# Kernel optimization log

Hardware: AMD Instinct MI355X
Metric: run time of the kernel (lower is better)

Reference implementation:

```python
import jax, jax.numpy as jnp
import numpy as np

N_NODES = 100000
N_EDGES = 3200000
F_IN, HIDDEN, NCLASS = 512, 256, 40


def setup_inputs() -> dict:
    key = jax.random.key(0)
    k1, k2, k3, k4, k5, k6 = jax.random.split(key, 6)
    x = jax.random.normal(k1, (N_NODES, F_IN), dtype=jnp.float32)
    edge_row = jax.random.randint(k2, (N_EDGES,), 0, N_NODES, dtype=jnp.int32)
    edge_col = jax.random.randint(k3, (N_EDGES,), 0, N_NODES, dtype=jnp.int32)
    edge_vals = jax.random.uniform(k4, (N_EDGES,), dtype=jnp.float32)
    stdv1 = 1.0 / np.sqrt(HIDDEN)
    stdv2 = 1.0 / np.sqrt(NCLASS)
    W1 = jax.random.uniform(k5, (F_IN, HIDDEN), minval=-stdv1, maxval=stdv1, dtype=jnp.float32)
    W2 = jax.random.uniform(k6, (HIDDEN, NCLASS), minval=-stdv2, maxval=stdv2, dtype=jnp.float32)
    return {"x": x, "edge_row": edge_row, "edge_col": edge_col,
            "edge_vals": edge_vals, "W1": W1, "W2": W2}


def _spmm(edge_row, edge_col, edge_vals, dense):
    # out[r] = sum_{edges e with row r} vals[e] * dense[col[e]]
    msgs = edge_vals[:, None] * dense[edge_col]  # [E, D]
    return jax.ops.segment_sum(msgs, edge_row, num_segments=N_NODES)


def reference(x, edge_row, edge_col, edge_vals, W1, W2):
    # Layer 1: dense projection + sparse aggregation + ReLU
    h = jax.nn.relu(_spmm(edge_row, edge_col, edge_vals, x @ W1))  # [N, HIDDEN]
    # dropout is identity in eval mode
    # Layer 2
    h = jax.nn.relu(_spmm(edge_row, edge_col, edge_vals, h @ W2))  # [N, NCLASS]
    return jax.nn.log_softmax(h, axis=1)
```

## Files before the change

kernel.cpp:

```cpp
#include <hip/hip_runtime.h>
#include <math.h>

#define N_NODES 100000
#define N_EDGES 3200000
#define F_IN    512
#define HIDDEN  256
#define NCLASS  40
#define NPAD    48
#define H2STRIDE 64
#define FB_ROWS 16
#define G1_BLOCKS ((N_NODES + 63) / 64)
#define FILL_BLOCKS (N_EDGES / 256)

#define SCAN_B  256
#define N_SCANB ((N_NODES + SCAN_B - 1) / SCAN_B)

typedef __attribute__((ext_vector_type(8))) _Float16 half8;
typedef __attribute__((ext_vector_type(4))) _Float16 half4;
typedef __attribute__((ext_vector_type(4))) float    f32x4;
typedef __attribute__((ext_vector_type(2))) float    f32x2;

__device__ __forceinline__ float unpack_val(unsigned pk) {
    unsigned short hb = (unsigned short)(pk & 0x7FFFu);
    _Float16 h = *(_Float16*)&hb;
    return (float)h;
}

__global__ __launch_bounds__(256) void init_kernel(const float* __restrict__ W1,
                                                   const float* __restrict__ W2,
                                                   _Float16* __restrict__ W1T,
                                                   _Float16* __restrict__ W2T,
                                                   int* __restrict__ deg) {
    int o = blockIdx.x * 256 + threadIdx.x;
    {
        int n = o >> 9, k = o & 511;
        W1T[o] = (_Float16)W1[(size_t)k * HIDDEN + n];
    }
    if (o < NPAD * HIDDEN) {
        int n = o >> 8, k = o & 255;
        W2T[o] = (n < NCLASS) ? (_Float16)W2[(size_t)k * NCLASS + n] : (_Float16)0.f;
    }
    if (o < N_NODES) deg[o] = 0;
}

__global__ __launch_bounds__(256) void hist2_kernel(const int* __restrict__ erow,
                                                    int* __restrict__ deg,
                                                    unsigned short* __restrict__ ke, int E) {
    int e = blockIdx.x * 256 + threadIdx.x;
    if (e < E) ke[e] = (unsigned short)atomicAdd(&deg[erow[e]], 1);
}

__global__ __launch_bounds__(256) void scanA_kernel(const int* __restrict__ deg,
                                                    int* __restrict__ rptr,
                                                    int* __restrict__ bsum, int n) {
    __shared__ int s[SCAN_B];
    int i = blockIdx.x * SCAN_B + threadIdx.x;
    int v = (i < n) ? deg[i] : 0;
    s[threadIdx.x] = v;
    __syncthreads();
    #pragma unroll
    for (int off = 1; off < SCAN_B; off <<= 1) {
        int t = (threadIdx.x >= off) ? s[threadIdx.x - off] : 0;
        __syncthreads();
        s[threadIdx.x] += t;
        __syncthreads();
    }
    if (i < n) rptr[i] = s[threadIdx.x] - v;
    if (threadIdx.x == SCAN_B - 1) bsum[blockIdx.x] = s[SCAN_B - 1];
}

__global__ __launch_bounds__(512) void scanB_kernel(int* __restrict__ bsum, int nb) {
    __shared__ int s[512];
    int t = threadIdx.x;
    int v = (t < nb) ? bsum[t] : 0;
    s[t] = v;
    __syncthreads();
    #pragma unroll
    for (int off = 1; off < 512; off <<= 1) {
        int x = (t >= off) ? s[t - off] : 0;
        __syncthreads();
        s[t] += x;
        __syncthreads();
    }
    if (t < nb) bsum[t] = s[t] - v;
}

__global__ __launch_bounds__(256) void scanC_kernel(int* __restrict__ rptr,
                                                    const int* __restrict__ bsum,
                                                    int n, int E) {
    int i = blockIdx.x * SCAN_B + threadIdx.x;
    if (i < n) rptr[i] += bsum[blockIdx.x];
    if (i == 0) rptr[n] = E;
}

__global__ __launch_bounds__(256) void fill_gemm1_kernel(
        const float* __restrict__ A, const _Float16* __restrict__ BT,
        unsigned char* __restrict__ C, int M,
        const int* __restrict__ erow, const int* __restrict__ ecol,
        const float* __restrict__ evals, const int* __restrict__ rptr,
        const unsigned short* __restrict__ ke, unsigned* __restrict__ cvp, int E) {
    __shared__ __align__(16) char smem[33792];

    if (blockIdx.x >= G1_BLOCKS) {
        int e = (blockIdx.x - G1_BLOCKS) * 256 + threadIdx.x;
        if (e < E) {
            int p = rptr[erow[e]] + ke[e];
            _Float16 h = (_Float16)evals[e];
            unsigned short hb = *(unsigned short*)&h;
            cvp[p] = ((unsigned)ecol[e] << 15) | (unsigned)(hb & 0x7FFFu);
        }
        return;
    }

    _Float16 (*As)[40]  = (_Float16 (*)[40])smem;
    _Float16 (*Bs)[40]  = (_Float16 (*)[40])(smem + 5120);
    _Float16 (*sC)[264] = (_Float16 (*)[264])smem;

    const int t    = threadIdx.x;
    const int m0   = blockIdx.x * 64;
    const int lane = t & 63;
    const int wid  = t >> 6;
    const int lr   = lane & 15, lk = lane >> 4;

    f32x4 acc[4][4] = {};

    const int  ar   = t >> 2;
    const int  aq   = t & 3;
    const bool aval = (m0 + ar) < M;
    const float*    aptr = A  + (size_t)(m0 + ar) * F_IN + aq * 8;
    const _Float16* bptr = BT + (size_t)t * F_IN;

    float4 a0 = {0.f,0.f,0.f,0.f}, a1 = {0.f,0.f,0.f,0.f};
    half8 b0, b1, b2, b3;
    if (aval) { a0 = *(const float4*)(aptr); a1 = *(const float4*)(aptr + 4); }
    { const half8* bp = (const half8*)(bptr); b0 = bp[0]; b1 = bp[1]; b2 = bp[2]; b3 = bp[3]; }

    for (int k0 = 0; k0 < F_IN; k0 += 32) {
        half8 ah;
        ah[0]=(_Float16)a0.x; ah[1]=(_Float16)a0.y; ah[2]=(_Float16)a0.z; ah[3]=(_Float16)a0.w;
        ah[4]=(_Float16)a1.x; ah[5]=(_Float16)a1.y; ah[6]=(_Float16)a1.z; ah[7]=(_Float16)a1.w;
        *(half8*)&As[ar][aq * 8] = ah;
        *(half8*)&Bs[t][0]  = b0;
        *(half8*)&Bs[t][8]  = b1;
        *(half8*)&Bs[t][16] = b2;
        *(half8*)&Bs[t][24] = b3;
        __syncthreads();

        if (k0 + 32 < F_IN) {
            if (aval) {
                a0 = *(const float4*)(aptr + k0 + 32);
                a1 = *(const float4*)(aptr + k0 + 36);
            }
            const half8* bp = (const half8*)(bptr + k0 + 32);
            b0 = bp[0]; b1 = bp[1]; b2 = bp[2]; b3 = bp[3];
        }

        half8 af[4], bf[4];
        #pragma unroll
        for (int fm = 0; fm < 4; fm++) af[fm] = *(half8*)&As[fm * 16 + lr][lk * 8];
        #pragma unroll
        for (int fn = 0; fn < 4; fn++) bf[fn] = *(half8*)&Bs[wid * 64 + fn * 16 + lr][lk * 8];
        #pragma unroll
        for (int fm = 0; fm < 4; fm++)
            #pragma unroll
            for (int fn = 0; fn < 4; fn++)
                acc[fm][fn] = __builtin_amdgcn_mfma_f32_16x16x32_f16(af[fm], bf[fn], acc[fm][fn], 0, 0, 0);
        __syncthreads();
    }

    #pragma unroll
    for (int fm = 0; fm < 4; fm++)
        #pragma unroll
        for (int fn = 0; fn < 4; fn++)
            #pragma unroll
            for (int j = 0; j < 4; j++) {
                int row = fm * 16 + lk * 4 + j;
                int col = wid * 64 + fn * 16 + lr;
                sC[row][col] = (_Float16)acc[fm][fn][j];
            }
    __syncthreads();

    int m = m0 + ar;
    if (m < M) {
        const half8* sp = (const half8*)&sC[ar][aq * 64];
        unsigned w[16];
        #pragma unroll
        for (int c = 0; c < 8; c++) {
            half8 hv = sp[c];
            unsigned lo = __builtin_amdgcn_cvt_pk_fp8_f32((float)hv[0], (float)hv[1], 0u, false);
            lo = __builtin_amdgcn_cvt_pk_fp8_f32((float)hv[2], (float)hv[3], lo, true);
            unsigned hi = __builtin_amdgcn_cvt_pk_fp8_f32((float)hv[4], (float)hv[5], 0u, false);
            hi = __builtin_amdgcn_cvt_pk_fp8_f32((float)hv[6], (float)hv[7], hi, true);
            w[c * 2]     = lo;
            w[c * 2 + 1] = hi;
        }
        uint4* dp = (uint4*)(C + (size_t)m * HIDDEN + aq * 64);
        #pragma unroll
        for (int c = 0; c < 4; c++)
            dp[c] = make_uint4(w[c*4], w[c*4+1], w[c*4+2], w[c*4+3]);
    }
}

__global__ __launch_bounds__(1024) void spmm_gemm2_kernel(const int* __restrict__ rptr,
                                                          const unsigned* __restrict__ cvp,
                                                          const unsigned char* __restrict__ H1,
                                                          const _Float16* __restrict__ W2T,
                                                          _Float16* __restrict__ H2) {
    __shared__ _Float16 sW2[NPAD][264];
    __shared__ _Float16 sRow[16][264];

    int t = threadIdx.x;
    int wave = t >> 6, lane = t & 63;
    int m0 = blockIdx.x * FB_ROWS;
    int r = m0 + wave;

    #pragma unroll
    for (int i = 0; i < 2; i++) {
        int idx = t + i * 1024;
        if (idx < NPAD * 32) {
            int row = idx >> 5, c8 = idx & 31;
            *(half8*)&sW2[row][c8 * 8] = *(const half8*)(W2T + (size_t)row * HIDDEN + c8 * 8);
        }
    }

    int e0 = rptr[r], e1 = rptr[r + 1];
    int qf = lane >> 4;
    int fl = lane & 15;

    float acc[16] = {};
    for (int e = e0; e < e1; e += 16) {
        #pragma unroll
        for (int u = 0; u < 4; u++) {
            int idx = e + 4 * u + qf;
            bool ok = idx < e1;
            unsigned pk = cvp[ok ? idx : (e1 - 1)];
            float v = ok ? unpack_val(pk) : 0.f;
            int col = (int)(pk >> 15);
            uint4 raw = *(const uint4*)(H1 + (size_t)col * HIDDEN + fl * 16);
            #pragma unroll
            for (int q = 0; q < 4; q++) {
                unsigned wq = (q == 0) ? raw.x : (q == 1) ? raw.y : (q == 2) ? raw.z : raw.w;
                f32x2 lo = __builtin_amdgcn_cvt_pk_f32_fp8(wq, false);
                f32x2 hi = __builtin_amdgcn_cvt_pk_f32_fp8(wq, true);
                acc[q*4 + 0] += v * lo[0];
                acc[q*4 + 1] += v * lo[1];
                acc[q*4 + 2] += v * hi[0];
                acc[q*4 + 3] += v * hi[1];
            }
        }
    }
    #pragma unroll
    for (int j = 0; j < 16; j++) {
        acc[j] += __shfl_xor(acc[j], 32);
        acc[j] += __shfl_xor(acc[j], 16);
    }

    if (lane < 16) {
        half8 o0, o1;
        #pragma unroll
        for (int j = 0; j < 8; j++) {
            o0[j] = (_Float16)fmaxf(acc[j], 0.f);
            o1[j] = (_Float16)fmaxf(acc[8 + j], 0.f);
        }
        *(half8*)&sRow[wave][fl * 16]     = o0;
        *(half8*)&sRow[wave][fl * 16 + 8] = o1;
    }
    __syncthreads();

    if (wave == 0) {
        int lr = lane & 15, lk = lane >> 4;
        f32x4 acc2[3] = {};
        #pragma unroll
        for (int ks = 0; ks < 8; ks++) {
            half8 af = *(half8*)&sRow[lr][ks * 32 + lk * 8];
            #pragma unroll
            for (int fn = 0; fn < 3; fn++) {
                half8 bf = *(half8*)&sW2[fn * 16 + lr][ks * 32 + lk * 8];
                acc2[fn] = __builtin_amdgcn_mfma_f32_16x16x32_f16(af, bf, acc2[fn], 0, 0, 0);
            }
        }
        #pragma unroll
        for (int fn = 0; fn < 3; fn++)
            #pragma unroll
            for (int j = 0; j < 4; j++) {
                int row = lk * 4 + j;
                int col = fn * 16 + lr;
                H2[(size_t)(m0 + row) * H2STRIDE + col] = (_Float16)acc2[fn][j];
            }
    }
}

__global__ __launch_bounds__(256) void spmm40_ls_kernel(const int* __restrict__ rptr,
                                                        const unsigned* __restrict__ cvp,
                                                        const _Float16* __restrict__ H2,
                                                        float* __restrict__ out) {
    int t = threadIdx.x;
    int wave = t >> 6, lane = t & 63;
    int r = blockIdx.x * 4 + wave;

    int e0 = rptr[r], e1 = rptr[r + 1];
    int s = lane / 5;
    int g = lane % 5;
    bool lact = lane < 60;

    float acc[8] = {};
    for (int e = e0; e < e1; e += 24) {
        int idx0 = e + s, idx1 = e + 12 + s;
        bool ok0 = lact && (idx0 < e1);
        bool ok1 = lact && (idx1 < e1);
        unsigned pk0 = cvp[ok0 ? idx0 : (e1 - 1)];
        unsigned pk1 = cvp[ok1 ? idx1 : (e1 - 1)];
        float v0 = ok0 ? unpack_val(pk0) : 0.f;
        float v1 = ok1 ? unpack_val(pk1) : 0.f;
        int c0 = (int)(pk0 >> 15), c1 = (int)(pk1 >> 15);
        half8 h0 = *(const half8*)(H2 + (size_t)c0 * H2STRIDE + g * 8);
        half8 h1 = *(const half8*)(H2 + (size_t)c1 * H2STRIDE + g * 8);
        #pragma unroll
        for (int j = 0; j < 8; j++)
            acc[j] += v0 * (float)h0[j] + v1 * (float)h1[j];
    }

    #pragma unroll
    for (int j = 0; j < 8; j++) acc[j] += __shfl(acc[j], lane + 30);
    #pragma unroll
    for (int j = 0; j < 8; j++) acc[j] += __shfl(acc[j], lane + 15);
    #pragma unroll
    for (int j = 0; j < 8; j++) {
        float t1 = __shfl(acc[j], lane + 5);
        float t2 = __shfl(acc[j], lane + 10);
        acc[j] += t1 + t2;
    }

    bool act = lane < 5;
    float z[8];
    float mx = -INFINITY;
    #pragma unroll
    for (int j = 0; j < 8; j++) {
        z[j] = act ? fmaxf(acc[j], 0.f) : -INFINITY;
        mx = fmaxf(mx, z[j]);
    }
    mx = fmaxf(mx, __shfl_xor(mx, 1));
    mx = fmaxf(mx, __shfl_xor(mx, 2));
    mx = fmaxf(mx, __shfl_xor(mx, 4));

    float sm = 0.f;
    #pragma unroll
    for (int j = 0; j < 8; j++)
        sm += act ? expf(z[j] - mx) : 0.f;
    sm += __shfl_xor(sm, 1);
    sm += __shfl_xor(sm, 2);
    sm += __shfl_xor(sm, 4);

    float lse = logf(sm);
    if (act) {
        float4 o0 = {z[0]-mx-lse, z[1]-mx-lse, z[2]-mx-lse, z[3]-mx-lse};
        float4 o1 = {z[4]-mx-lse, z[5]-mx-lse, z[6]-mx-lse, z[7]-mx-lse};
        float4* dp = (float4*)(out + (size_t)r * NCLASS + g * 8);
        dp[0] = o0;
        dp[1] = o1;
    }
}

extern "C" void kernel_launch(void* const* d_in, const int* in_sizes, int n_in,
                              void* d_out, int out_size, void* d_ws, size_t ws_size,
                              hipStream_t stream) {
    const float* x     = (const float*)d_in[0];
    const int*   erow  = (const int*)d_in[1];
    const int*   ecol  = (const int*)d_in[2];
    const float* evals = (const float*)d_in[3];
    const float* W1    = (const float*)d_in[4];
    const float* W2    = (const float*)d_in[5];
    float* out = (float*)d_out;

    const int M = N_NODES;
    const int E = N_EDGES;

    char* p = (char*)d_ws;
    auto alloc = [&](size_t bytes) {
        char* q = p;
        p += (bytes + 255) & ~(size_t)255;
        return q;
    };
    int*            deg  = (int*)alloc(sizeof(int) * N_NODES);
    int*            rptr = (int*)alloc(sizeof(int) * (N_NODES + 1));
    int*            bsum = (int*)alloc(sizeof(int) * 512);
    unsigned short* ke   = (unsigned short*)alloc(sizeof(unsigned short) * N_EDGES);
    unsigned*       cvp  = (unsigned*)alloc(sizeof(unsigned) * N_EDGES);
    _Float16*       W1T  = (_Float16*)alloc(sizeof(_Float16) * F_IN * HIDDEN);
    _Float16*       W2T  = (_Float16*)alloc(sizeof(_Float16) * NPAD * HIDDEN);
    unsigned char*  H1   = (unsigned char*)alloc((size_t)N_NODES * HIDDEN);
    _Float16*       H2   = (_Float16*)alloc(sizeof(_Float16) * (size_t)N_NODES * H2STRIDE);

    init_kernel<<<(F_IN * HIDDEN) / 256, 256, 0, stream>>>(W1, W2, W1T, W2T, deg);

    hist2_kernel<<<E / 256, 256, 0, stream>>>(erow, deg, ke, E);

    scanA_kernel<<<N_SCANB, SCAN_B, 0, stream>>>(deg, rptr, bsum, N_NODES);
    scanB_kernel<<<1, 512, 0, stream>>>(bsum, N_SCANB);
    scanC_kernel<<<N_SCANB, SCAN_B, 0, stream>>>(rptr, bsum, N_NODES, E);

    fill_gemm1_kernel<<<G1_BLOCKS + FILL_BLOCKS, 256, 0, stream>>>(
        x, W1T, H1, M, erow, ecol, evals, rptr, ke, cvp, E);

    spmm_gemm2_kernel<<<M / FB_ROWS, 1024, 0, stream>>>(rptr, cvp, H1, W2T, H2);

    spmm40_ls_kernel<<<M / 4, 256, 0, stream>>>(rptr, cvp, H2, out);
}
```

Measured before the change: 518.2 us.

## Merge edge fill into GEMM1 blocks and halve epilogue shared-memory footprint

The separate edge-fill blocks are removed. Each GEMM1 block now also scatters 2048 edges into the CSR array after its tile, which cuts the grid to G1_BLOCKS (1563 blocks x 2048 edges covers all 3.2M edges). The output epilogue is split into two 32-row passes so shared memory drops from 33792 to 25600 bytes, and launch_bounds asks for 6 blocks per CU to raise occupancy. The cost is a serialized scatter tail inside each GEMM block and extra barriers, and the register cap could cause spills.

Result: slower. 794.5 us (+53.3%).

```diff
diff --git a/kernel.cpp b/kernel.cpp
--- a/kernel.cpp
+++ b/kernel.cpp
@@ -10,7 +10,7 @@
 #define H2STRIDE 64
 #define FB_ROWS 16
 #define G1_BLOCKS ((N_NODES + 63) / 64)
-#define FILL_BLOCKS (N_EDGES / 256)
+#define EDGES_PER_BLOCK 2048
 
 #define SCAN_B  256
 #define N_SCANB ((N_NODES + SCAN_B - 1) / SCAN_B)
@@ -93,25 +93,13 @@
     if (i == 0) rptr[n] = E;
 }
 
-__global__ __launch_bounds__(256) void fill_gemm1_kernel(
+__global__ __launch_bounds__(256, 6) void fill_gemm1_kernel(
         const float* __restrict__ A, const _Float16* __restrict__ BT,
         unsigned char* __restrict__ C, int M,
         const int* __restrict__ erow, const int* __restrict__ ecol,
         const float* __restrict__ evals, const int* __restrict__ rptr,
         const unsigned short* __restrict__ ke, unsigned* __restrict__ cvp, int E) {
-    __shared__ __align__(16) char smem[33792];
-
-    if (blockIdx.x >= G1_BLOCKS) {
-        int e = (blockIdx.x - G1_BLOCKS) * 256 + threadIdx.x;
-        if (e < E) {
-            int p = rptr[erow[e]] + ke[e];
-            _Float16 h = (_Float16)evals[e];
-            unsigned short hb = *(unsigned short*)&h;
-            cvp[p] = ((unsigned)ecol[e] << 15) | (unsigned)(hb & 0x7FFFu);
-        }
-        return;
-    }
-
+    __shared__ __align__(16) char smem[25600];
     _Float16 (*As)[40]  = (_Float16 (*)[40])smem;
     _Float16 (*Bs)[40]  = (_Float16 (*)[40])(smem + 5120);
     _Float16 (*sC)[264] = (_Float16 (*)[264])smem;
@@ -169,35 +157,54 @@
     }
 
     #pragma unroll
-    for (int fm = 0; fm < 4; fm++)
-        #pragma unroll
-        for (int fn = 0; fn < 4; fn++)
-            #pragma unroll
-            for (int j = 0; j < 4; j++) {
-                int row = fm * 16 + lk * 4 + j;
-                int col = wid * 64 + fn * 16 + lr;
-                sC[row][col] = (_Float16)acc[fm][fn][j];
+    for (int pass = 0; pass < 2; pass++) {
+        #pragma unroll
+        for (int fm = 0; fm < 2; fm++) {
+            int fmg = pass * 2 + fm;
+            #pragma unroll
+            for (int fn = 0; fn < 4; fn++)
+                #pragma unroll
+                for (int j = 0; j < 4; j++) {
+                    int row = fm * 16 + lk * 4 + j;
+                    int col = wid * 64 + fn * 16 + lr;
+                    sC[row][col] = (_Float16)acc[fmg][fn][j];
+                }
+        }
+        __syncthreads();
+
+        int row = t >> 3;
+        int c   = t & 7;
+        int m   = m0 + pass * 32 + row;
+        if (m < M) {
+            const half8* sp = (const half8*)&sC[row][c * 32];
+            unsigned w[8];
+            #pragma unroll
+            for (int cc = 0; cc < 4; cc++) {
+                half8 hv = sp[cc];
+                unsigned lo = __builtin_amdgcn_cvt_pk_fp8_f32((float)hv[0], (float)hv[1], 0u, false);
+                lo = __builtin_amdgcn_cvt_pk_fp8_f32((float)hv[2], (float)hv[3], lo, true);
+                unsigned hi = __builtin_amdgcn_cvt_pk_fp8_f32((float)hv[4], (float)hv[5], 0u, false);
+                hi = __builtin_amdgcn_cvt_pk_fp8_f32((float)hv[6], (float)hv[7], hi, true);
+                w[cc * 2]     = lo;
+                w[cc * 2 + 1] = hi;
             }
-    __syncthreads();
-
-    int m = m0 + ar;
-    if (m < M) {
-        const half8* sp = (const half8*)&sC[ar][aq * 64];
-        unsigned w[16];
-        #pragma unroll
-        for (int c = 0; c < 8; c++) {
-            half8 hv = sp[c];
-            unsigned lo = __builtin_amdgcn_cvt_pk_fp8_f32((float)hv[0], (float)hv[1], 0u, false);
-            lo = __builtin_amdgcn_cvt_pk_fp8_f32((float)hv[2], (float)hv[3], lo, true);
-            unsigned hi = __builtin_amdgcn_cvt_pk_fp8_f32((float)hv[4], (float)hv[5], 0u, false);
-            hi = __builtin_amdgcn_cvt_pk_fp8_f32((float)hv[6], (float)hv[7], hi, true);
-            w[c * 2]     = lo;
-            w[c * 2 + 1] = hi;
-        }
-        uint4* dp = (uint4*)(C + (size_t)m * HIDDEN + aq * 64);
-        #pragma unroll
-        for (int c = 0; c < 4; c++)
-            dp[c] = make_uint4(w[c*4], w[c*4+1], w[c*4+2], w[c*4+3]);
+            uint4* dp = (uint4*)(C + (size_t)m * HIDDEN + c * 32);
+            dp[0] = make_uint4(w[0], w[1], w[2], w[3]);
+            dp[1] = make_uint4(w[4], w[5], w[6], w[7]);
+        }
+        __syncthreads();
+    }
+
+    int ebase = blockIdx.x * EDGES_PER_BLOCK;
+    #pragma unroll
+    for (int i = 0; i < 8; i++) {
+        int e = ebase + i * 256 + t;
+        if (e < E) {
+            int p = rptr[erow[e]] + ke[e];
+            _Float16 h = (_Float16)evals[e];
+            unsigned short hb = *(unsigned short*)&h;
+            cvp[p] = ((unsigned)ecol[e] << 15) | (unsigned)(hb & 0x7FFFu);
+        }
     }
 }
 
@@ -399,7 +406,7 @@
     scanB_kernel<<<1, 512, 0, stream>>>(bsum, N_SCANB);
     scanC_kernel<<<N_SCANB, SCAN_B, 0, stream>>>(rptr, bsum, N_NODES, E);
 
-    fill_gemm1_kernel<<<G1_BLOCKS + FILL_BLOCKS, 256, 0, stream>>>(
+    fill_gemm1_kernel<<<G1_BLOCKS, 256, 0, stream>>>(
         x, W1T, H1, M, erow, ecol, evals, rptr, ke, cvp, E);
 
     spmm_gemm2_kernel<<<M / FB_ROWS, 1024, 0, stream>>>(rptr, cvp, H1, W2T, H2);
```
